# Kernel tuning notes

Hardware: AMD Instinct MI355X
Metric: run time of the kernel (lower is better)

The kernel has to match this reference:

```python
import jax, jax.numpy as jnp
import numpy as np

EPS = 1e-6
B, T, E, H = 2, 512, 1024, 256
NUM_BLOCK = 12


def normalize(x):
    # RMS-style normalization over the feature dim (no learned affine)
    return x * jax.lax.rsqrt(jnp.mean(x * x, axis=-1, keepdims=True) + EPS)


def bar_quadratic_causal(a, b):
    # y_i = (1/i) * sum_{j<=i} relu(a_i + b_j)   (causal prefix mean of pairwise relation)
    # a, b: [B, T, H]
    Tn = a.shape[1]
    pair = jax.nn.relu(a[:, :, None, :] + b[:, None, :, :])  # [B, T(i), T(j), H]
    mask = jnp.tril(jnp.ones((Tn, Tn), dtype=a.dtype))        # causal j<=i
    s = jnp.einsum('bijh,ij->bih', pair, mask)
    counts = jnp.arange(1, Tn + 1, dtype=a.dtype)[None, :, None]
    return s / counts


def setup_inputs() -> dict:
    key = jax.random.key(0)
    k0, k1, k2, k3 = jax.random.split(key, 4)
    x = jax.random.normal(k0, (B, T, E), dtype=jnp.float32)
    w1 = jax.random.normal(k1, (E, H), dtype=jnp.float32) * 0.02
    b1 = jnp.zeros((H,), dtype=jnp.float32)
    w2 = jax.random.normal(k2, (E, H), dtype=jnp.float32) * 0.02
    b2 = jnp.zeros((H,), dtype=jnp.float32)
    w3 = jax.random.normal(k3, (H, E), dtype=jnp.float32) * (0.02 / np.sqrt(NUM_BLOCK))
    b3 = jnp.zeros((E,), dtype=jnp.float32)
    return {"x": x, "w1": w1, "b1": b1, "w2": w2, "b2": b2, "w3": w3, "b3": b3}


def reference(x, w1, b1, w2, b2, w3, b3):
    r = normalize(x)
    a = r @ w1 + b1
    b = r @ w2 + b2
    # PreNorm == 'approx': normalize a and b separately
    a = normalize(a)
    b = normalize(b)
    r = bar_quadratic_causal(a, b)
    # PostNorm == 'yes'
    r = normalize(r)
    r = r @ w3 + b3
    return x + r
```

## Files before the change

kernel.cpp:

```cpp
#include <hip/hip_runtime.h>

#define EPSF 1e-6f
#define Bsz 2
#define Tn  512
#define En  1024
#define Hn  256
#define Mtot (Bsz * Tn)
typedef unsigned short us_t;
typedef unsigned int   u32_t;

typedef __attribute__((ext_vector_type(8))) short bf16x8;
typedef __attribute__((ext_vector_type(4))) float f32x4;
#define MFMA16(a, b, c) __builtin_amdgcn_mfma_f32_16x16x32_bf16((a), (b), (c), 0, 0, 0)

__device__ __forceinline__ us_t f2bf(float f) {
  union { float f; u32_t u; } x; x.f = f;
  u32_t r = (x.u + 0x7fffu + ((x.u >> 16) & 1u)) >> 16;
  return (us_t)r;
}
__device__ __forceinline__ float bf2f(us_t u) {
  union { u32_t u; float f; } x; x.u = ((u32_t)u) << 16; return x.f;
}
__device__ __forceinline__ uint2 pack4bf(float a, float b, float c, float d) {
  uint2 r;
  r.x = (u32_t)f2bf(a) | ((u32_t)f2bf(b) << 16);
  r.y = (u32_t)f2bf(c) | ((u32_t)f2bf(d) << 16);
  return r;
}
__device__ __forceinline__ float block_reduce_sum_256(float v, float* smem) {
  #pragma unroll
  for (int off = 32; off > 0; off >>= 1) v += __shfl_down(v, off, 64);
  const int wave = threadIdx.x >> 6;
  if ((threadIdx.x & 63) == 0) smem[wave] = v;
  __syncthreads();
  float s = smem[0] + smem[1] + smem[2] + smem[3];
  __syncthreads();
  return s;
}

__global__ __launch_bounds__(256) void k_castx_rs(
    const float* __restrict__ x, us_t* __restrict__ xb, float* __restrict__ rs)
{
  __shared__ float red[4];
  const int row = blockIdx.x, t = threadIdx.x;
  float4 v = ((const float4*)(x + (size_t)row * En))[t];
  float ss = block_reduce_sum_256(v.x*v.x + v.y*v.y + v.z*v.z + v.w*v.w, red);
  if (t == 0) rs[row] = rsqrtf(ss * (1.0f / En) + EPSF);
  ((uint2*)(xb + (size_t)row * En))[t] = pack4bf(v.x, v.y, v.z, v.w);
}

__global__ __launch_bounds__(256) void k_tr(
    const float* __restrict__ w1, const float* __restrict__ w2,
    const float* __restrict__ w3,
    us_t* __restrict__ w1t, us_t* __restrict__ w2t, us_t* __restrict__ w3t)
{
  const int b = blockIdx.x, t = threadIdx.x;
  const float* src; us_t* dst; int R, C, tr, tc;
  if (b < 256)      { src = w1; dst = w1t; R = 1024; C = 256;  tr = b >> 3;  tc = b & 7; }
  else if (b < 512) { int i = b - 256; src = w2; dst = w2t; R = 1024; C = 256; tr = i >> 3; tc = i & 7; }
  else              { int i = b - 512; src = w3; dst = w3t; R = 256; C = 1024; tr = i >> 5; tc = i & 31; }

  __shared__ float ts[32][33];
  const int r = t >> 3, c4 = (t & 7) * 4;
  float4 v = *(const float4*)(src + (size_t)(tr * 32 + r) * C + tc * 32 + c4);
  ts[r][c4 + 0] = v.x; ts[r][c4 + 1] = v.y; ts[r][c4 + 2] = v.z; ts[r][c4 + 3] = v.w;
  __syncthreads();
  float o0 = ts[c4 + 0][r], o1 = ts[c4 + 1][r], o2 = ts[c4 + 2][r], o3 = ts[c4 + 3][r];
  *(uint2*)(dst + (size_t)(tc * 32 + r) * R + tr * 32 + c4) = pack4bf(o0, o1, o2, o3);
}

__global__ __launch_bounds__(256) void k_gemm_ab(
    const us_t* __restrict__ xb,
    const us_t* __restrict__ w1t, const us_t* __restrict__ w2t,
    float* __restrict__ P)
{
  const int wid = threadIdx.x >> 6, lane = threadIdx.x & 63;
  const int wg = blockIdx.x * 4 + wid;
  const int ks = wg & 3, nt = (wg >> 2) & 15, mt = wg >> 6;
  const int m0 = mt * 32, n0 = nt * 32, k0 = ks * 256;
  const int lg = lane >> 4, lr = lane & 15;

  const us_t* ap0 = xb + (size_t)(m0 + lr) * En + k0 + lg * 8;
  const us_t* ap1 = ap0 + 16 * En;
  const us_t* bbase = (n0 < Hn) ? (w1t + (size_t)n0 * En) : (w2t + (size_t)(n0 - Hn) * En);
  const us_t* bp0 = bbase + (size_t)lr * En + k0 + lg * 8;
  const us_t* bp1 = bp0 + 16 * En;

  f32x4 acc00 = {0.f,0.f,0.f,0.f}, acc01 = acc00, acc10 = acc00, acc11 = acc00;

  #pragma unroll 4
  for (int s = 0; s < 8; ++s) {
    bf16x8 a0 = *(const bf16x8*)(ap0 + s * 32);
    bf16x8 a1 = *(const bf16x8*)(ap1 + s * 32);
    bf16x8 b0 = *(const bf16x8*)(bp0 + s * 32);
    bf16x8 b1 = *(const bf16x8*)(bp1 + s * 32);
    acc00 = MFMA16(a0, b0, acc00);
    acc01 = MFMA16(a0, b1, acc01);
    acc10 = MFMA16(a1, b0, acc10);
    acc11 = MFMA16(a1, b1, acc11);
  }

  float* pw = P + ((size_t)ks * Mtot + m0 + lg * 4) * 512 + n0 + lr;
  #pragma unroll
  for (int i = 0; i < 4; ++i) {
    pw[(size_t)i        * 512      ] = acc00[i];
    pw[(size_t)i        * 512 + 16 ] = acc01[i];
    pw[(size_t)(i + 16) * 512      ] = acc10[i];
    pw[(size_t)(i + 16) * 512 + 16 ] = acc11[i];
  }
}

__global__ __launch_bounds__(256) void k_norm(
    const float* __restrict__ P, const float* __restrict__ rs,
    const float* __restrict__ b1, const float* __restrict__ b2,
    us_t* __restrict__ A, us_t* __restrict__ Bm)
{
  const int rw = blockIdx.x * 4 + (threadIdx.x >> 6);
  const int lane = threadIdx.x & 63;
  const int which = rw >> 10, r = rw & 1023;
  const float* bias = which ? b2 : b1;
  const int h0 = lane * 4;
  const size_t off = (size_t)r * 512 + which * Hn + h0;
  const size_t KS = (size_t)Mtot * 512;

  float4 d0 = *(const float4*)(P + off);
  float4 d1 = *(const float4*)(P + off + KS);
  float4 d2 = *(const float4*)(P + off + 2 * KS);
  float4 d3 = *(const float4*)(P + off + 3 * KS);
  const float sc0 = rs[r];
  float4 bv = *(const float4*)(bias + h0);
  float vx = (d0.x + d1.x + d2.x + d3.x) * sc0 + bv.x;
  float vy = (d0.y + d1.y + d2.y + d3.y) * sc0 + bv.y;
  float vz = (d0.z + d1.z + d2.z + d3.z) * sc0 + bv.z;
  float vw = (d0.w + d1.w + d2.w + d3.w) * sc0 + bv.w;

  float ss = vx*vx + vy*vy + vz*vz + vw*vw;
  #pragma unroll
  for (int off2 = 32; off2 > 0; off2 >>= 1) ss += __shfl_xor(ss, off2, 64);
  const float sc = rsqrtf(ss * (1.0f / Hn) + EPSF);

  us_t* outp = which ? Bm : A;
  *(uint2*)(outp + (size_t)r * Hn + h0) = pack4bf(vx * sc, vy * sc, vz * sc, vw * sc);
}

#define ITILE 2
#define JCH   16
__global__ __launch_bounds__(256) void k_bar(
    const us_t* __restrict__ A, const us_t* __restrict__ Bm,
    us_t* __restrict__ Yb)
{
  const int tile = blockIdx.x & 255;
  const int bb   = blockIdx.x >> 8;
  const int i0   = tile * ITILE;
  const int h    = threadIdx.x;
  const size_t base = (size_t)bb * Tn * Hn;
  const us_t* __restrict__ bp = Bm + base + h;

  float av[ITILE], sum[ITILE];
  #pragma unroll
  for (int r = 0; r < ITILE; ++r) {
    av[r]  = bf2f(A[base + (size_t)(i0 + r) * Hn + h]);
    sum[r] = 0.f;
  }

  const int nfull = i0 & ~(JCH - 1);
  us_t b0[JCH], b1[JCH];

  #define LOADCH(buf, jj) { _Pragma("unroll") \
    for (int tt = 0; tt < JCH; ++tt) buf[tt] = bp[(size_t)((jj) + tt) * Hn]; }
  #define COMPCH(buf) { _Pragma("unroll") \
    for (int tt = 0; tt < JCH; ++tt) { float bv = bf2f(buf[tt]); _Pragma("unroll") \
      for (int r = 0; r < ITILE; ++r) sum[r] += fmaxf(av[r] + bv, 0.f); } }

  if (nfull > 0) {
    LOADCH(b0, 0);
    int j = 0;
    while (true) {
      const bool more1 = (j + JCH     < nfull);
      const bool more2 = (j + 2 * JCH < nfull);
      if (more1) LOADCH(b1, j + JCH);
      COMPCH(b0);
      j += JCH;
      if (!more1) break;
      if (more2) LOADCH(b0, j + JCH);
      COMPCH(b1);
      j += JCH;
      if (!more2) break;
    }
  }
  {
    us_t bt[JCH];
    LOADCH(bt, nfull);
    const int lim = i0 - nfull;
    #pragma unroll
    for (int tt = 0; tt < JCH; ++tt) {
      float bv = bf2f(bt[tt]);
      #pragma unroll
      for (int r = 0; r < ITILE; ++r)
        sum[r] += (tt <= lim + r) ? fmaxf(av[r] + bv, 0.f) : 0.f;
    }
  }
  #undef LOADCH
  #undef COMPCH

  __shared__ float red[4];
  #pragma unroll
  for (int r = 0; r < ITILE; ++r) {
    float ss = block_reduce_sum_256(sum[r] * sum[r], red);
    float c  = (float)(i0 + r + 1);
    float sc = rsqrtf(ss * (1.0f / Hn) + EPSF * c * c);
    Yb[base + (size_t)(i0 + r) * Hn + h] = f2bf(sum[r] * sc);
  }
}

__global__ __launch_bounds__(256) void k_out(
    const us_t* __restrict__ Yb, const us_t* __restrict__ w3t,
    const float* __restrict__ x, const float* __restrict__ b3,
    float* __restrict__ out)
{
  const int wid = threadIdx.x >> 6, lane = threadIdx.x & 63;
  const int wg = blockIdx.x * 4 + wid;
  const int nt = wg & 31, mt = wg >> 5;
  const int m0 = mt * 16, n0 = nt * 32;
  const int lg = lane >> 4, lr = lane & 15;

  const us_t* ap  = Yb  + (size_t)(m0 + lr) * Hn + lg * 8;
  const us_t* bp0 = w3t + (size_t)(n0 + lr) * Hn + lg * 8;
  const us_t* bp1 = bp0 + 16 * Hn;

  f32x4 acc0 = {0.f,0.f,0.f,0.f}, acc1 = acc0;

  #pragma unroll 4
  for (int s = 0; s < 8; ++s) {
    bf16x8 a  = *(const bf16x8*)(ap  + s * 32);
    bf16x8 b0 = *(const bf16x8*)(bp0 + s * 32);
    bf16x8 b1 = *(const bf16x8*)(bp1 + s * 32);
    acc0 = MFMA16(a, b0, acc0);
    acc1 = MFMA16(a, b1, acc1);
  }

  const int row = m0 + lg * 4;
  const int c0 = n0 + lr, c1 = n0 + 16 + lr;
  const float bv0 = b3[c0], bv1 = b3[c1];
  #pragma unroll
  for (int i = 0; i < 4; ++i) {
    const size_t o0 = (size_t)(row + i) * En + c0;
    const size_t o1 = (size_t)(row + i) * En + c1;
    out[o0] = x[o0] + acc0[i] + bv0;
    out[o1] = x[o1] + acc1[i] + bv1;
  }
}

extern "C" void kernel_launch(void* const* d_in, const int* in_sizes, int n_in,
                              void* d_out, int out_size, void* d_ws, size_t ws_size,
                              hipStream_t stream) {
  const float* x  = (const float*)d_in[0];
  const float* w1 = (const float*)d_in[1];
  const float* b1 = (const float*)d_in[2];
  const float* w2 = (const float*)d_in[3];
  const float* b2 = (const float*)d_in[4];
  const float* w3 = (const float*)d_in[5];
  const float* b3 = (const float*)d_in[6];
  float* out = (float*)d_out;

  char* p = (char*)d_ws;
  float* P   = (float*)p;               p += (size_t)4 * Mtot * 512 * 4;
  us_t* xb   = (us_t*)p;                p += (size_t)Mtot * En * 2;
  us_t* w1t  = (us_t*)p;                p += (size_t)Hn * En * 2;
  us_t* w2t  = (us_t*)p;                p += (size_t)Hn * En * 2;
  us_t* w3t  = (us_t*)p;                p += (size_t)En * Hn * 2;
  us_t* A    = (us_t*)p;                p += (size_t)Mtot * Hn * 2;
  us_t* Bm   = (us_t*)p;                p += (size_t)Mtot * Hn * 2;
  us_t* Yb   = (us_t*)p;                p += (size_t)Mtot * Hn * 2;
  float* rs  = (float*)p;               p += (size_t)Mtot * 4;

  k_castx_rs<<<Mtot, 256, 0, stream>>>(x, xb, rs);
  k_tr      <<<768,  256, 0, stream>>>(w1, w2, w3, w1t, w2t, w3t);
  k_gemm_ab <<<512,  256, 0, stream>>>(xb, w1t, w2t, P);
  k_norm    <<<512,  256, 0, stream>>>(P, rs, b1, b2, A, Bm);
  k_bar     <<<Bsz * (Tn / ITILE), 256, 0, stream>>>(A, Bm, Yb);
  k_out     <<<512,  256, 0, stream>>>(Yb, w3t, x, b3, out);
}
```

Baseline: 53.30 us.

## Fuse prep kernels, reduce split-K in LDS, transpose B for vectorized causal loop

Merges the x cast/rms and weight transpose kernels into one launch. The first GEMM now does its split-K reduction in shared memory inside each block, so the 4x partial buffer and its readback in the norm kernel go away. The norm kernel writes B transposed (H-major), which lets the causal pairwise kernel load 8 bf16 values per vector read instead of strided scalar loads. The causal kernel also pairs light and heavy row tiles across blocks to balance load, and launch bounds and unrolls are adjusted. The cost is strided 2-byte scattered writes for the transposed B.

```diff
diff --git a/kernel.cpp b/kernel.cpp
--- a/kernel.cpp
+++ b/kernel.cpp
@@ -38,29 +38,43 @@
   return s;
 }
 
-__global__ __launch_bounds__(256) void k_castx_rs(
-    const float* __restrict__ x, us_t* __restrict__ xb, float* __restrict__ rs)
-{
-  __shared__ float red[4];
-  const int row = blockIdx.x, t = threadIdx.x;
-  float4 v = ((const float4*)(x + (size_t)row * En))[t];
-  float ss = block_reduce_sum_256(v.x*v.x + v.y*v.y + v.z*v.z + v.w*v.w, red);
-  if (t == 0) rs[row] = rsqrtf(ss * (1.0f / En) + EPSF);
-  ((uint2*)(xb + (size_t)row * En))[t] = pack4bf(v.x, v.y, v.z, v.w);
-}
-
-__global__ __launch_bounds__(256) void k_tr(
+__global__ __launch_bounds__(256) void k_prep(
+    const float* __restrict__ x,
     const float* __restrict__ w1, const float* __restrict__ w2,
     const float* __restrict__ w3,
+    us_t* __restrict__ xb, float* __restrict__ rs,
     us_t* __restrict__ w1t, us_t* __restrict__ w2t, us_t* __restrict__ w3t)
 {
   const int b = blockIdx.x, t = threadIdx.x;
+
+  if (b < 256) {
+    const int wid = t >> 6, lane = t & 63;
+    const int row = b * 4 + wid;
+    const float4* xp = (const float4*)(x + (size_t)row * En);
+    float4 v[4];
+    #pragma unroll
+    for (int i = 0; i < 4; ++i) v[i] = xp[lane + 64 * i];
+    float ss = 0.f;
+    #pragma unroll
+    for (int i = 0; i < 4; ++i)
+      ss += v[i].x*v[i].x + v[i].y*v[i].y + v[i].z*v[i].z + v[i].w*v[i].w;
+    #pragma unroll
+    for (int off = 32; off > 0; off >>= 1) ss += __shfl_xor(ss, off, 64);
+    if (lane == 0) rs[row] = rsqrtf(ss * (1.0f / En) + EPSF);
+    uint2* xo = (uint2*)(xb + (size_t)row * En);
+    #pragma unroll
+    for (int i = 0; i < 4; ++i)
+      xo[lane + 64 * i] = pack4bf(v[i].x, v[i].y, v[i].z, v[i].w);
+    return;
+  }
+
+  __shared__ float ts[32][33];
+  const int i = b - 256;
   const float* src; us_t* dst; int R, C, tr, tc;
-  if (b < 256)      { src = w1; dst = w1t; R = 1024; C = 256;  tr = b >> 3;  tc = b & 7; }
-  else if (b < 512) { int i = b - 256; src = w2; dst = w2t; R = 1024; C = 256; tr = i >> 3; tc = i & 7; }
-  else              { int i = b - 512; src = w3; dst = w3t; R = 256; C = 1024; tr = i >> 5; tc = i & 31; }
-
-  __shared__ float ts[32][33];
+  if (i < 256)      { src = w1; dst = w1t; R = 1024; C = 256;  tr = i >> 3;  tc = i & 7; }
+  else if (i < 512) { int k = i - 256; src = w2; dst = w2t; R = 1024; C = 256; tr = k >> 3; tc = k & 7; }
+  else              { int k = i - 512; src = w3; dst = w3t; R = 256; C = 1024; tr = k >> 5; tc = k & 31; }
+
   const int r = t >> 3, c4 = (t & 7) * 4;
   float4 v = *(const float4*)(src + (size_t)(tr * 32 + r) * C + tc * 32 + c4);
   ts[r][c4 + 0] = v.x; ts[r][c4 + 1] = v.y; ts[r][c4 + 2] = v.z; ts[r][c4 + 3] = v.w;
@@ -69,151 +83,165 @@
   *(uint2*)(dst + (size_t)(tc * 32 + r) * R + tr * 32 + c4) = pack4bf(o0, o1, o2, o3);
 }
 
-__global__ __launch_bounds__(256) void k_gemm_ab(
+__global__ __launch_bounds__(256, 4) void k_gemm(
     const us_t* __restrict__ xb,
     const us_t* __restrict__ w1t, const us_t* __restrict__ w2t,
-    float* __restrict__ P)
-{
+    float* __restrict__ Praw)
+{
+  const int blk = blockIdx.x;
+  const int mt = blk >> 4, nt = blk & 15;
+  const int m0 = mt * 16, n0 = nt * 32;
   const int wid = threadIdx.x >> 6, lane = threadIdx.x & 63;
-  const int wg = blockIdx.x * 4 + wid;
-  const int ks = wg & 3, nt = (wg >> 2) & 15, mt = wg >> 6;
-  const int m0 = mt * 32, n0 = nt * 32, k0 = ks * 256;
   const int lg = lane >> 4, lr = lane & 15;
-
-  const us_t* ap0 = xb + (size_t)(m0 + lr) * En + k0 + lg * 8;
-  const us_t* ap1 = ap0 + 16 * En;
-  const us_t* bbase = (n0 < Hn) ? (w1t + (size_t)n0 * En) : (w2t + (size_t)(n0 - Hn) * En);
+  const int k0 = wid * 256;
+
+  const us_t* ap = xb + (size_t)(m0 + lr) * En + k0 + lg * 8;
+  const us_t* bbase = (n0 < Hn) ? (w1t + (size_t)n0 * En)
+                                : (w2t + (size_t)(n0 - Hn) * En);
   const us_t* bp0 = bbase + (size_t)lr * En + k0 + lg * 8;
-  const us_t* bp1 = bp0 + 16 * En;
-
-  f32x4 acc00 = {0.f,0.f,0.f,0.f}, acc01 = acc00, acc10 = acc00, acc11 = acc00;
-
-  #pragma unroll 4
+  const us_t* bp1 = bp0 + (size_t)16 * En;
+
+  f32x4 acc0 = {0.f,0.f,0.f,0.f}, acc1 = acc0;
+
+  #pragma unroll
   for (int s = 0; s < 8; ++s) {
-    bf16x8 a0 = *(const bf16x8*)(ap0 + s * 32);
-    bf16x8 a1 = *(const bf16x8*)(ap1 + s * 32);
+    bf16x8 a  = *(const bf16x8*)(ap  + s * 32);
     bf16x8 b0 = *(const bf16x8*)(bp0 + s * 32);
     bf16x8 b1 = *(const bf16x8*)(bp1 + s * 32);
-    acc00 = MFMA16(a0, b0, acc00);
-    acc01 = MFMA16(a0, b1, acc01);
-    acc10 = MFMA16(a1, b0, acc10);
-    acc11 = MFMA16(a1, b1, acc11);
-  }
-
-  float* pw = P + ((size_t)ks * Mtot + m0 + lg * 4) * 512 + n0 + lr;
+    acc0 = MFMA16(a, b0, acc0);
+    acc1 = MFMA16(a, b1, acc1);
+  }
+
+  __shared__ float cmb[4][16][32];
   #pragma unroll
   for (int i = 0; i < 4; ++i) {
-    pw[(size_t)i        * 512      ] = acc00[i];
-    pw[(size_t)i        * 512 + 16 ] = acc01[i];
-    pw[(size_t)(i + 16) * 512      ] = acc10[i];
-    pw[(size_t)(i + 16) * 512 + 16 ] = acc11[i];
+    cmb[wid][lg * 4 + i][lr]      = acc0[i];
+    cmb[wid][lg * 4 + i][16 + lr] = acc1[i];
+  }
+  __syncthreads();
+
+  #pragma unroll
+  for (int e = 0; e < 2; ++e) {
+    const int idx = threadIdx.x + e * 256;
+    const int row = idx >> 5, col = idx & 31;
+    float s = cmb[0][row][col] + cmb[1][row][col]
+            + cmb[2][row][col] + cmb[3][row][col];
+    Praw[(size_t)(m0 + row) * 512 + n0 + col] = s;
   }
 }
 
 __global__ __launch_bounds__(256) void k_norm(
-    const float* __restrict__ P, const float* __restrict__ rs,
+    const float* __restrict__ Praw, const float* __restrict__ rs,
     const float* __restrict__ b1, const float* __restrict__ b2,
-    us_t* __restrict__ A, us_t* __restrict__ Bm)
+    us_t* __restrict__ A, us_t* __restrict__ BmT)
 {
   const int rw = blockIdx.x * 4 + (threadIdx.x >> 6);
   const int lane = threadIdx.x & 63;
   const int which = rw >> 10, r = rw & 1023;
+  const int h0 = lane * 4;
+
+  float4 d = *(const float4*)(Praw + (size_t)r * 512 + which * Hn + h0);
+  const float s0 = rs[r];
   const float* bias = which ? b2 : b1;
-  const int h0 = lane * 4;
-  const size_t off = (size_t)r * 512 + which * Hn + h0;
-  const size_t KS = (size_t)Mtot * 512;
-
-  float4 d0 = *(const float4*)(P + off);
-  float4 d1 = *(const float4*)(P + off + KS);
-  float4 d2 = *(const float4*)(P + off + 2 * KS);
-  float4 d3 = *(const float4*)(P + off + 3 * KS);
-  const float sc0 = rs[r];
   float4 bv = *(const float4*)(bias + h0);
-  float vx = (d0.x + d1.x + d2.x + d3.x) * sc0 + bv.x;
-  float vy = (d0.y + d1.y + d2.y + d3.y) * sc0 + bv.y;
-  float vz = (d0.z + d1.z + d2.z + d3.z) * sc0 + bv.z;
-  float vw = (d0.w + d1.w + d2.w + d3.w) * sc0 + bv.w;
+  float vx = d.x * s0 + bv.x, vy = d.y * s0 + bv.y;
+  float vz = d.z * s0 + bv.z, vw = d.w * s0 + bv.w;
 
   float ss = vx*vx + vy*vy + vz*vz + vw*vw;
   #pragma unroll
-  for (int off2 = 32; off2 > 0; off2 >>= 1) ss += __shfl_xor(ss, off2, 64);
+  for (int o2 = 32; o2 > 0; o2 >>= 1) ss += __shfl_xor(ss, o2, 64);
   const float sc = rsqrtf(ss * (1.0f / Hn) + EPSF);
 
-  us_t* outp = which ? Bm : A;
-  *(uint2*)(outp + (size_t)r * Hn + h0) = pack4bf(vx * sc, vy * sc, vz * sc, vw * sc);
-}
-
-#define ITILE 2
-#define JCH   16
+  if (!which) {
+    *(uint2*)(A + (size_t)r * Hn + h0) = pack4bf(vx*sc, vy*sc, vz*sc, vw*sc);
+  } else {
+    const int bb = r >> 9, tcol = r & 511;
+    us_t* bt = BmT + (size_t)bb * Hn * Tn + tcol;
+    bt[(size_t)(h0 + 0) * Tn] = f2bf(vx * sc);
+    bt[(size_t)(h0 + 1) * Tn] = f2bf(vy * sc);
+    bt[(size_t)(h0 + 2) * Tn] = f2bf(vz * sc);
+    bt[(size_t)(h0 + 3) * Tn] = f2bf(vw * sc);
+  }
+}
+
+#define JCHB 32
 __global__ __launch_bounds__(256) void k_bar(
-    const us_t* __restrict__ A, const us_t* __restrict__ Bm,
+    const us_t* __restrict__ A, const us_t* __restrict__ BmT,
     us_t* __restrict__ Yb)
 {
-  const int tile = blockIdx.x & 255;
-  const int bb   = blockIdx.x >> 8;
-  const int i0   = tile * ITILE;
-  const int h    = threadIdx.x;
-  const size_t base = (size_t)bb * Tn * Hn;
-  const us_t* __restrict__ bp = Bm + base + h;
-
-  float av[ITILE], sum[ITILE];
-  #pragma unroll
-  for (int r = 0; r < ITILE; ++r) {
-    av[r]  = bf2f(A[base + (size_t)(i0 + r) * Hn + h]);
-    sum[r] = 0.f;
-  }
-
-  const int nfull = i0 & ~(JCH - 1);
-  us_t b0[JCH], b1[JCH];
-
-  #define LOADCH(buf, jj) { _Pragma("unroll") \
-    for (int tt = 0; tt < JCH; ++tt) buf[tt] = bp[(size_t)((jj) + tt) * Hn]; }
-  #define COMPCH(buf) { _Pragma("unroll") \
-    for (int tt = 0; tt < JCH; ++tt) { float bv = bf2f(buf[tt]); _Pragma("unroll") \
-      for (int r = 0; r < ITILE; ++r) sum[r] += fmaxf(av[r] + bv, 0.f); } }
+  const int raw = blockIdx.x;
+  const int sel = (raw < 256) ? raw : (511 - raw);
+  const int bb  = raw >> 8;
+  const int i0  = sel * 2;
+  const int h   = threadIdx.x;
+  const size_t baseA = (size_t)bb * Tn * Hn;
+  const us_t* __restrict__ bt = BmT + (size_t)bb * Hn * Tn + (size_t)h * Tn;
+
+  float av0 = bf2f(A[baseA + (size_t)i0 * Hn + h]);
+  float av1 = bf2f(A[baseA + (size_t)(i0 + 1) * Hn + h]);
+  float sum0 = 0.f, sum1 = 0.f;
+
+  const int nfull = i0 & ~(JCHB - 1);
+  bf16x8 c0[4], c1[4];
+
+  #define LOADC(dst, jj) { _Pragma("unroll") \
+    for (int q = 0; q < 4; ++q) dst[q] = *(const bf16x8*)(bt + (jj) + q * 8); }
+  #define PROCF(srcb) { _Pragma("unroll") \
+    for (int q = 0; q < 4; ++q) { _Pragma("unroll") \
+      for (int e = 0; e < 8; ++e) { \
+        float bv = bf2f((us_t)srcb[q][e]); \
+        sum0 += fmaxf(av0 + bv, 0.f); \
+        sum1 += fmaxf(av1 + bv, 0.f); } } }
 
   if (nfull > 0) {
-    LOADCH(b0, 0);
+    LOADC(c0, 0);
     int j = 0;
     while (true) {
-      const bool more1 = (j + JCH     < nfull);
-      const bool more2 = (j + 2 * JCH < nfull);
-      if (more1) LOADCH(b1, j + JCH);
-      COMPCH(b0);
-      j += JCH;
-      if (!more1) break;
-      if (more2) LOADCH(b0, j + JCH);
-      COMPCH(b1);
-      j += JCH;
-      if (!more2) break;
+      const bool m1 = (j + JCHB     < nfull);
+      const bool m2 = (j + 2 * JCHB < nfull);
+      if (m1) LOADC(c1, j + JCHB);
+      PROCF(c0);
+      j += JCHB;
+      if (!m1) break;
+      if (m2) LOADC(c0, j + JCHB);
+      PROCF(c1);
+      j += JCHB;
+      if (!m2) break;
     }
   }
   {
-    us_t bt[JCH];
-    LOADCH(bt, nfull);
+    bf16x8 ct[4];
+    LOADC(ct, nfull);
     const int lim = i0 - nfull;
     #pragma unroll
-    for (int tt = 0; tt < JCH; ++tt) {
-      float bv = bf2f(bt[tt]);
+    for (int q = 0; q < 4; ++q)
       #pragma unroll
-      for (int r = 0; r < ITILE; ++r)
-        sum[r] += (tt <= lim + r) ? fmaxf(av[r] + bv, 0.f) : 0.f;
-    }
-  }
-  #undef LOADCH
-  #undef COMPCH
+      for (int e = 0; e < 8; ++e) {
+        const int jl = q * 8 + e;
+        float bv = bf2f((us_t)ct[q][e]);
+        sum0 += (jl <= lim)     ? fmaxf(av0 + bv, 0.f) : 0.f;
+        sum1 += (jl <= lim + 1) ? fmaxf(av1 + bv, 0.f) : 0.f;
+      }
+  }
+  #undef LOADC
+  #undef PROCF
 
   __shared__ float red[4];
-  #pragma unroll
-  for (int r = 0; r < ITILE; ++r) {
-    float ss = block_reduce_sum_256(sum[r] * sum[r], red);
-    float c  = (float)(i0 + r + 1);
+  {
+    float ss = block_reduce_sum_256(sum0 * sum0, red);
+    float c  = (float)(i0 + 1);
     float sc = rsqrtf(ss * (1.0f / Hn) + EPSF * c * c);
-    Yb[base + (size_t)(i0 + r) * Hn + h] = f2bf(sum[r] * sc);
-  }
-}
-
-__global__ __launch_bounds__(256) void k_out(
+    Yb[baseA + (size_t)i0 * Hn + h] = f2bf(sum0 * sc);
+  }
+  {
+    float ss = block_reduce_sum_256(sum1 * sum1, red);
+    float c  = (float)(i0 + 2);
+    float sc = rsqrtf(ss * (1.0f / Hn) + EPSF * c * c);
+    Yb[baseA + (size_t)(i0 + 1) * Hn + h] = f2bf(sum1 * sc);
+  }
+}
+
+__global__ __launch_bounds__(256, 4) void k_out(
     const us_t* __restrict__ Yb, const us_t* __restrict__ w3t,
     const float* __restrict__ x, const float* __restrict__ b3,
     float* __restrict__ out)
@@ -226,11 +254,11 @@
 
   const us_t* ap  = Yb  + (size_t)(m0 + lr) * Hn + lg * 8;
   const us_t* bp0 = w3t + (size_t)(n0 + lr) * Hn + lg * 8;
-  const us_t* bp1 = bp0 + 16 * Hn;
+  const us_t* bp1 = bp0 + (size_t)16 * Hn;
 
   f32x4 acc0 = {0.f,0.f,0.f,0.f}, acc1 = acc0;
 
-  #pragma unroll 4
+  #pragma unroll
   for (int s = 0; s < 8; ++s) {
     bf16x8 a  = *(const bf16x8*)(ap  + s * 32);
     bf16x8 b0 = *(const bf16x8*)(bp0 + s * 32);
@@ -263,21 +291,20 @@
   const float* b3 = (const float*)d_in[6];
   float* out = (float*)d_out;
 
-  char* p = (char*)d_ws;
-  float* P   = (float*)p;               p += (size_t)4 * Mtot * 512 * 4;
-  us_t* xb   = (us_t*)p;                p += (size_t)Mtot * En * 2;
-  us_t* w1t  = (us_t*)p;                p += (size_t)Hn * En * 2;
-  us_t* w2t  = (us_t*)p;                p += (size_t)Hn * En * 2;
-  us_t* w3t  = (us_t*)p;                p += (size_t)En * Hn * 2;
-  us_t* A    = (us_t*)p;                p += (size_t)Mtot * Hn * 2;
-  us_t* Bm   = (us_t*)p;                p += (size_t)Mtot * Hn * 2;
-  us_t* Yb   = (us_t*)p;                p += (size_t)Mtot * Hn * 2;
-  float* rs  = (float*)p;               p += (size_t)Mtot * 4;
-
-  k_castx_rs<<<Mtot, 256, 0, stream>>>(x, xb, rs);
-  k_tr      <<<768,  256, 0, stream>>>(w1, w2, w3, w1t, w2t, w3t);
-  k_gemm_ab <<<512,  256, 0, stream>>>(xb, w1t, w2t, P);
-  k_norm    <<<512,  256, 0, stream>>>(P, rs, b1, b2, A, Bm);
-  k_bar     <<<Bsz * (Tn / ITILE), 256, 0, stream>>>(A, Bm, Yb);
-  k_out     <<<512,  256, 0, stream>>>(Yb, w3t, x, b3, out);
-}
+  char* q = (char*)d_ws;
+  float* Praw = (float*)q;  q += (size_t)Mtot * 512 * 4;
+  us_t* xb    = (us_t*)q;   q += (size_t)Mtot * En * 2;
+  us_t* w1t   = (us_t*)q;   q += (size_t)Hn * En * 2;
+  us_t* w2t   = (us_t*)q;   q += (size_t)Hn * En * 2;
+  us_t* w3t   = (us_t*)q;   q += (size_t)En * Hn * 2;
+  us_t* A     = (us_t*)q;   q += (size_t)Mtot * Hn * 2;
+  us_t* BmT   = (us_t*)q;   q += (size_t)Mtot * Hn * 2;
+  us_t* Yb    = (us_t*)q;   q += (size_t)Mtot * Hn * 2;
+  float* rs   = (float*)q;  q += (size_t)Mtot * 4;
+
+  k_prep<<<1024, 256, 0, stream>>>(x, w1, w2, w3, xb, rs, w1t, w2t, w3t);
+  k_gemm<<<1024, 256, 0, stream>>>(xb, w1t, w2t, Praw);
+  k_norm<<<512,  256, 0, stream>>>(Praw, rs, b1, b2, A, BmT);
+  k_bar <<<512,  256, 0, stream>>>(A, BmT, Yb);
+  k_out <<<512,  256, 0, stream>>>(Yb, w3t, x, b3, out);
+}
```

Result: faster. 47.64 us (-10.6%).
